# Performance work log

Measured on AMD Instinct MI355X. Metric: run time of the kernel, lower is better.

Reference implementation:

```python
import jax, jax.numpy as jnp
import numpy as np

EPS = 1e-8
PHI = (1 + 5 ** 0.5) / 2
B, S, D, H, L, O = 8, 2048, 256, 512, 3, 1
NH = 4
HD = H // NH


def setup_inputs() -> dict:
    key = jax.random.key(0)
    ks = jax.random.split(key, 12)
    g = lambda k, shape, s=0.02: jax.random.normal(k, shape, dtype=jnp.float32) * s
    # Fibonacci modular spiral embedding (fixed, requires_grad=False in torch)
    idx = jnp.arange(D, dtype=jnp.float32)
    r = (PHI * idx) % 1.0
    th = 2 * jnp.pi * r
    phase_emb = jnp.stack([r * jnp.cos(th), r * jnp.sin(th)], axis=1)  # [D,2]
    return dict(
        x=jax.random.normal(ks[0], (B, S, D), dtype=jnp.float32),
        proj_w=g(ks[1], (D, D), 0.06), proj_b=jnp.zeros((D,), jnp.float32),
        phase_emb=phase_emb,
        hebb_w=g(ks[2], (H, 2), 0.5),
        attn_in_w=g(ks[3], (L, 3 * H, H)), attn_in_b=jnp.zeros((L, 3 * H), jnp.float32),
        attn_out_w=g(ks[4], (L, H, H)), attn_out_b=jnp.zeros((L, H), jnp.float32),
        ff1_w=g(ks[5], (L, 4 * H, H)), ff1_b=jnp.zeros((L, 4 * H), jnp.float32),
        ff2_w=g(ks[6], (L, H, 4 * H)), ff2_b=jnp.zeros((L, H), jnp.float32),
        ln1_w=jnp.ones((L, H), jnp.float32), ln1_b=jnp.zeros((L, H), jnp.float32),
        ln2_w=jnp.ones((L, H), jnp.float32), ln2_b=jnp.zeros((L, H), jnp.float32),
        normA_w=jnp.ones((H,), jnp.float32), normA_b=jnp.zeros((H,), jnp.float32),
        normB_w=jnp.ones((H // 2,), jnp.float32), normB_b=jnp.zeros((H // 2,), jnp.float32),
        p1_w=g(ks[7], (H // 2, H), 0.04), p1_b=jnp.zeros((H // 2,), jnp.float32),
        p2_w=g(ks[8], (O, H // 2), 0.06), p2_b=jnp.zeros((O,), jnp.float32),
    )


def _ln(x, w, b, eps=1e-5):
    m = x.mean(-1, keepdims=True)
    v = ((x - m) ** 2).mean(-1, keepdims=True)
    return (x - m) * jax.lax.rsqrt(v + eps) * w + b


def _diffuse(psi, mask, dt, steps):
    # Norm-preserving RK2 integration of d(psi)/dt = mask@psi - psi
    def force(state):
        return jnp.einsum('bij,bjd->bid', mask, state) - state

    def step(p, _):
        r = jnp.linalg.norm(p, axis=-1, keepdims=True)
        k1 = force(p)
        ps = p + dt * k1
        ps = ps * (r / (jnp.linalg.norm(ps, axis=-1, keepdims=True) + EPS))
        k2 = force(ps)
        pn = p + 0.5 * dt * (k1 + k2)
        pn = pn * (r / (jnp.linalg.norm(pn, axis=-1, keepdims=True) + EPS))
        return pn, None

    psi, _ = jax.lax.scan(step, psi, None, length=steps)
    return psi


def _forward(x, proj_w, proj_b, phase_emb, hebb_w, attn_in_w, attn_in_b,
             attn_out_w, attn_out_b, ff1_w, ff1_b, ff2_w, ff2_b,
             ln1_w, ln1_b, ln2_w, ln2_b, normA_w, normA_b, normB_w, normB_b,
             p1_w, p1_b, p2_w, p2_b):
    b, s, _ = x.shape
    # PhaseHebbianEmbedder: project then map to 2D phase coords, unit-normalize
    xp = x @ proj_w.T + proj_b                               # [B,S,D]
    pc = jnp.einsum('bsd,dt->bst', xp, phase_emb)            # [B,S,2]
    psi = pc / (jnp.linalg.norm(pc, axis=-1, keepdims=True) + EPS)
    mask = jnp.broadcast_to(jnp.eye(s, dtype=x.dtype), (b, s, s))  # [B,S,S]
    psi = _diffuse(psi, mask, 0.1, 3)
    psi = _diffuse(psi, mask, 0.05, 4)
    A = jnp.einsum('bsd,btd->bst', psi, psi)                 # [B,S,S]
    final_psi = psi[:, -1]                                   # [B,2]
    h = (final_psi @ hebb_w.T)[:, None, :]                   # [B,1,H]
    for l in range(attn_in_w.shape[0]):
        qkv = h @ attn_in_w[l].T + attn_in_b[l]
        q, k, v = jnp.split(qkv, 3, axis=-1)
        hd = lambda t: t.reshape(b, -1, NH, HD).transpose(0, 2, 1, 3)
        q, k, v = hd(q), hd(k), hd(v)
        sc = jnp.einsum('bhqd,bhkd->bhqk', q, k) / jnp.sqrt(jnp.float32(HD))
        att = jax.nn.softmax(sc, axis=-1)
        o = jnp.einsum('bhqk,bhkd->bhqd', att, v).transpose(0, 2, 1, 3).reshape(b, -1, H)
        o = o @ attn_out_w[l].T + attn_out_b[l]
        h = _ln(h + o, ln1_w[l], ln1_b[l])
        ff = jax.nn.silu(h @ ff1_w[l].T + ff1_b[l]) @ ff2_w[l].T + ff2_b[l]
        h = _ln(h + ff, ln2_w[l], ln2_b[l])
    h = _ln(h[:, 0, :], normA_w, normA_b)
    p = jax.nn.silu(h @ p1_w.T + p1_b)
    p = _ln(p, normB_w, normB_b)
    preds = p @ p2_w.T + p2_b                                # [B,O]
    return preds, A, mask, psi


def reference(x, proj_w, proj_b, phase_emb, hebb_w, attn_in_w, attn_in_b,
              attn_out_w, attn_out_b, ff1_w, ff1_b, ff2_w, ff2_b,
              ln1_w, ln1_b, ln2_w, ln2_b, normA_w, normA_b, normB_w, normB_b,
              p1_w, p1_b, p2_w, p2_b):
    return _forward(x, proj_w, proj_b, phase_emb, hebb_w, attn_in_w, attn_in_b,
                    attn_out_w, attn_out_b, ff1_w, ff1_b, ff2_w, ff2_b,
                    ln1_w, ln1_b, ln2_w, ln2_b, normA_w, normA_b,
                    normB_w, normB_b, p1_w, p1_b, p2_w, p2_b)
```

## Files before the change

### kernel.cpp

```cpp
#include <hip/hip_runtime.h>
#include <hip/hip_bf16.h>

#define BB 8
#define SS 2048
#define DD 256
#define HH 512
#define LL 3

__global__ void compute_M(const float* __restrict__ pw, const float* __restrict__ pb,
                          const float* __restrict__ pe, float* __restrict__ Mc)
{
    int tid = threadIdx.x;
    int k = tid >> 2;
    int sub = tid & 3;
    float a0 = 0.f, a1 = 0.f;
    #pragma unroll 8
    for (int d = sub * 64; d < sub * 64 + 64; ++d) {
        float w = pw[d * DD + k];
        a0 += w * pe[2 * d];
        a1 += w * pe[2 * d + 1];
    }
    a0 += __shfl_xor(a0, 1); a0 += __shfl_xor(a0, 2);
    a1 += __shfl_xor(a1, 1); a1 += __shfl_xor(a1, 2);
    if (sub == 0) {
        Mc[2 * k] = a0;
        Mc[2 * k + 1] = a1;
    }
    if (tid == 0) {
        float c0 = 0.f, c1 = 0.f;
        #pragma unroll 4
        for (int d = 0; d < DD; ++d) {
            c0 += pb[d] * pe[2 * d];
            c1 += pb[d] * pe[2 * d + 1];
        }
        Mc[512] = c0;
        Mc[513] = c1;
    }
}

__global__ void psi_kernel(const float* __restrict__ x, const float* __restrict__ Mc,
                           float* __restrict__ psi)
{
    __shared__ float sM[516];
    int tid = threadIdx.x;
    for (int i = tid; i < 514; i += 256) sM[i] = Mc[i];
    __syncthreads();

    int sub = tid & 3;
    int rloc = tid >> 2;
    int rid = blockIdx.x * 64 + rloc;
    const float4* xr = reinterpret_cast<const float4*>(x + (size_t)rid * DD);
    float a0 = 0.f, a1 = 0.f;
    #pragma unroll
    for (int i = sub; i < DD / 4; i += 4) {
        float4 v = xr[i];
        int k2 = i * 8;
        a0 += v.x * sM[k2]     + v.y * sM[k2 + 2] + v.z * sM[k2 + 4] + v.w * sM[k2 + 6];
        a1 += v.x * sM[k2 + 1] + v.y * sM[k2 + 3] + v.z * sM[k2 + 5] + v.w * sM[k2 + 7];
    }
    a0 += __shfl_xor(a0, 1); a0 += __shfl_xor(a0, 2);
    a1 += __shfl_xor(a1, 1); a1 += __shfl_xor(a1, 2);

    if (sub == 0) {
        a0 += sM[512];
        a1 += sM[513];
        float n = sqrtf(a0 * a0 + a1 * a1);
        float scale = 1.f / (n + 1e-8f);
        float r = n * scale;
        #pragma unroll
        for (int it = 0; it < 7; ++it) {
            float f = r / (r + 1e-8f);
            scale *= f;
            r *= f;
        }
        float2 pv;
        pv.x = a0 * scale;
        pv.y = a1 * scale;
        *reinterpret_cast<float2*>(psi + (size_t)rid * 2) = pv;
    }
}

__global__ void h0_kernel(const float* __restrict__ psi, const float* __restrict__ hebb,
                          float* __restrict__ h0)
{
    int b = blockIdx.x;
    int j = threadIdx.x;
    float2 pv = *reinterpret_cast<const float2*>(psi + ((size_t)b * SS + SS - 1) * 2);
    h0[(size_t)b * HH + j] = pv.x * hebb[2 * j] + pv.y * hebb[2 * j + 1];
}

__global__ void a_mask_kernel(const float* __restrict__ psi,
                              float* __restrict__ A, float* __restrict__ M)
{
    int blk = blockIdx.x;
    int b = blk >> 11, i = blk & (SS - 1);
    int tid = threadIdx.x;
    float2 pi = *reinterpret_cast<const float2*>(psi + (size_t)blk * 2);
    #pragma unroll
    for (int c = 0; c < 2; ++c) {
        int j0 = c * 1024 + tid * 4;
        const float4* pr = reinterpret_cast<const float4*>(psi + ((size_t)b * SS + j0) * 2);
        float4 q0 = pr[0], q1 = pr[1];
        float4 o;
        o.x = pi.x * q0.x + pi.y * q0.y;
        o.y = pi.x * q0.z + pi.y * q0.w;
        o.z = pi.x * q1.x + pi.y * q1.y;
        o.w = pi.x * q1.z + pi.y * q1.w;
        size_t rb = (size_t)blk * SS + j0;
        *reinterpret_cast<float4*>(A + rb) = o;
        float4 m;
        m.x = (i == j0    ) ? 1.f : 0.f;
        m.y = (i == j0 + 1) ? 1.f : 0.f;
        m.z = (i == j0 + 2) ? 1.f : 0.f;
        m.w = (i == j0 + 3) ? 1.f : 0.f;
        *reinterpret_cast<float4*>(M + rb) = m;
    }
}

__global__ void head_mm(const float* __restrict__ X, int K,
                        const float* __restrict__ xlnw, const float* __restrict__ xlnb,
                        const float* __restrict__ xln2w, const float* __restrict__ xln2b,
                        const float* __restrict__ W, const float* __restrict__ bias,
                        const float* __restrict__ res,
                        const float* __restrict__ reslnw, const float* __restrict__ reslnb,
                        float* __restrict__ out, int J, int G, int act)
{
    extern __shared__ float sX[];
    __shared__ float s_m[8], s_r[8], s_rm[8], s_rr[8];
    const int tid = threadIdx.x;
    const int row = tid >> 5, lane = tid & 31;
    const bool doLN = (xlnw != nullptr);
    const bool doRLN = (res != nullptr) && (reslnw != nullptr);

    if (doLN) {
        float s = 0.f, ss = 0.f;
        for (int k = lane; k < K; k += 32) {
            float v = X[row * K + k];
            s += v; ss += v * v;
        }
        for (int d = 16; d; d >>= 1) { s += __shfl_down(s, d); ss += __shfl_down(ss, d); }
        if (lane == 0) {
            float m = s / K;
            s_m[row] = m;
            s_r[row] = rsqrtf(ss / K - m * m + 1e-5f);
        }
    }
    if (doRLN) {
        float s = 0.f, ss = 0.f;
        for (int k = lane; k < J; k += 32) {
            float v = res[row * J + k];
            s += v; ss += v * v;
        }
        for (int d = 16; d; d >>= 1) { s += __shfl_down(s, d); ss += __shfl_down(ss, d); }
        if (lane == 0) {
            float m = s / J;
            s_rm[row] = m;
            s_rr[row] = rsqrtf(ss / J - m * m + 1e-5f);
        }
    }
    __syncthreads();

    if (doLN) {
        for (int idx = tid; idx < 8 * K; idx += 256) {
            int b = idx / K, k = idx - b * K;
            sX[idx] = (X[idx] - s_m[b]) * s_r[b] * xlnw[k] + xlnb[k];
        }
        __syncthreads();
        if (xln2w) {
            float s = 0.f, ss = 0.f;
            for (int k = lane; k < K; k += 32) {
                float v = sX[row * K + k];
                s += v; ss += v * v;
            }
            for (int d = 16; d; d >>= 1) { s += __shfl_down(s, d); ss += __shfl_down(ss, d); }
            if (lane == 0) {
                float m = s / K;
                s_m[row] = m;
                s_r[row] = rsqrtf(ss / K - m * m + 1e-5f);
            }
            __syncthreads();
            for (int idx = tid; idx < 8 * K; idx += 256) {
                int b = idx / K, k = idx - b * K;
                sX[idx] = (sX[idx] - s_m[b]) * s_r[b] * xln2w[k] + xln2b[k];
            }
            __syncthreads();
        }
    }

    const float* __restrict__ Xp = doLN ? (const float*)sX : X;
    const int g = tid & (G - 1);
    const int jj = tid / G;
    const int j = blockIdx.x * (256 / G) + jj;

    float acc[8] = {0.f, 0.f, 0.f, 0.f, 0.f, 0.f, 0.f, 0.f};
    if (j < J) {
        const float4* W4 = reinterpret_cast<const float4*>(W + (size_t)j * K);
        const int K4 = K >> 2;
        for (int i4 = g; i4 < K4; i4 += G) {
            float4 w4 = W4[i4];
            int k = i4 << 2;
            #pragma unroll
            for (int b = 0; b < 8; ++b) {
                float4 xv = *reinterpret_cast<const float4*>(Xp + b * K + k);
                acc[b] = fmaf(w4.x, xv.x, acc[b]);
                acc[b] = fmaf(w4.y, xv.y, acc[b]);
                acc[b] = fmaf(w4.z, xv.z, acc[b]);
                acc[b] = fmaf(w4.w, xv.w, acc[b]);
            }
        }
    }
    for (int d = G >> 1; d; d >>= 1) {
        #pragma unroll
        for (int b = 0; b < 8; ++b) acc[b] += __shfl_down(acc[b], d);
    }
    if (g == 0 && j < J) {
        float bs = bias ? bias[j] : 0.f;
        #pragma unroll
        for (int b = 0; b < 8; ++b) {
            float v = acc[b] + bs;
            if (act) v = v / (1.f + expf(-v));
            if (res) {
                float rv = res[(size_t)b * J + j];
                if (reslnw) rv = (rv - s_rm[b]) * s_rr[b] * reslnw[j] + reslnb[j];
                v += rv;
            }
            out[(size_t)b * J + j] = v;
        }
    }
}

extern "C" void kernel_launch(void* const* d_in, const int* in_sizes, int n_in,
                              void* d_out, int out_size, void* d_ws, size_t ws_size,
                              hipStream_t stream)
{
    const float* x      = (const float*)d_in[0];
    const float* proj_w = (const float*)d_in[1];
    const float* proj_b = (const float*)d_in[2];
    const float* pe     = (const float*)d_in[3];
    const float* hebb   = (const float*)d_in[4];
    const float* ai_w   = (const float*)d_in[5];
    const float* ai_b   = (const float*)d_in[6];
    const float* ao_w   = (const float*)d_in[7];
    const float* ao_b   = (const float*)d_in[8];
    const float* f1_w   = (const float*)d_in[9];
    const float* f1_b   = (const float*)d_in[10];
    const float* f2_w   = (const float*)d_in[11];
    const float* f2_b   = (const float*)d_in[12];
    const float* ln1w   = (const float*)d_in[13];
    const float* ln1b   = (const float*)d_in[14];
    const float* ln2w   = (const float*)d_in[15];
    const float* ln2b   = (const float*)d_in[16];
    const float* nAw    = (const float*)d_in[17];
    const float* nAb    = (const float*)d_in[18];
    const float* nBw    = (const float*)d_in[19];
    const float* nBb    = (const float*)d_in[20];
    const float* p1w    = (const float*)d_in[21];
    const float* p1b    = (const float*)d_in[22];
    const float* p2w    = (const float*)d_in[23];
    const float* p2b    = (const float*)d_in[24];

    float* out   = (float*)d_out;
    float* preds = out;
    float* A     = out + 8;
    float* Mask  = out + 8 + (size_t)BB * SS * SS;
    float* Psi   = out + 8 + (size_t)2 * BB * SS * SS;

    float* ws = (float*)d_ws;
    float* Mc = ws;
    float* T  = ws + 640;
    float* V  = ws + 4736;
    float* T1 = ws + 8832;
    float* F  = ws + 12928;
    float* P  = ws + 29312;

    compute_M<<<1, 1024, 0, stream>>>(proj_w, proj_b, pe, Mc);
    psi_kernel<<<(BB * SS) / 64, 256, 0, stream>>>(x, Mc, Psi);
    h0_kernel<<<BB, HH, 0, stream>>>(Psi, hebb, T);
    a_mask_kernel<<<BB * SS, 256, 0, stream>>>(Psi, A, Mask);

    for (int l = 0; l < LL; ++l) {
        const float* pxw = l ? ln2w + (l - 1) * HH : nullptr;
        const float* pxb = l ? ln2b + (l - 1) * HH : nullptr;
        head_mm<<<64, 256, (pxw ? 8 * HH * 4 : 0), stream>>>(
            T, HH, pxw, pxb, nullptr, nullptr,
            ai_w + ((size_t)l * 3 * HH + 2 * HH) * HH, ai_b + l * 3 * HH + 2 * HH,
            nullptr, nullptr, nullptr, V, HH, 32, 0);
        head_mm<<<64, 256, 0, stream>>>(
            V, HH, nullptr, nullptr, nullptr, nullptr,
            ao_w + (size_t)l * HH * HH, ao_b + l * HH,
            T, pxw, pxb, T1, HH, 32, 0);
        head_mm<<<128, 256, 8 * HH * 4, stream>>>(
            T1, HH, ln1w + l * HH, ln1b + l * HH, nullptr, nullptr,
            f1_w + (size_t)l * 4 * HH * HH, f1_b + l * 4 * HH,
            nullptr, nullptr, nullptr, F, 4 * HH, 16, 1);
        head_mm<<<128, 256, 0, stream>>>(
            F, 4 * HH, nullptr, nullptr, nullptr, nullptr,
            f2_w + (size_t)l * HH * 4 * HH, f2_b + l * HH,
            T1, ln1w + l * HH, ln1b + l * HH, T, HH, 64, 0);
    }
    head_mm<<<32, 256, 8 * HH * 4, stream>>>(
        T, HH, ln2w + 2 * HH, ln2b + 2 * HH, nAw, nAb,
        p1w, p1b, nullptr, nullptr, nullptr, P, HH / 2, 32, 1);
    head_mm<<<1, 256, 8 * (HH / 2) * 4, stream>>>(
        P, HH / 2, nBw, nBb, nullptr, nullptr,
        p2w, p2b, nullptr, nullptr, nullptr, preds, 1, 32, 0);
}
```

Measured before the change: 249.4 us.

## Spread A/mask row writes across head kernels as extra blocks

The standalone A/mask kernel is removed. Its 16384 rows are split into chunks of about 1092 rows, and each chunk runs as extra blocks appended to the h0 kernel and to every small head matmul launch. This lets the bandwidth-bound writes overlap the latency-bound tiny matmuls. psi_kernel now uses one wave per row with wave-wide shuffles, and compute_M reduces through shared memory. The risk is that the extra blocks delay the matmul blocks on the critical path.

```diff
diff --git a/kernel.cpp b/kernel.cpp
--- a/kernel.cpp
+++ b/kernel.cpp
@@ -6,95 +6,14 @@
 #define DD 256
 #define HH 512
 #define LL 3
-
-__global__ void compute_M(const float* __restrict__ pw, const float* __restrict__ pb,
-                          const float* __restrict__ pe, float* __restrict__ Mc)
+#define NROWS (BB * SS)
+
+__device__ __forceinline__ void amask_row(const float* __restrict__ psi,
+                                          float* __restrict__ A, float* __restrict__ M,
+                                          int blk)
 {
     int tid = threadIdx.x;
-    int k = tid >> 2;
-    int sub = tid & 3;
-    float a0 = 0.f, a1 = 0.f;
-    #pragma unroll 8
-    for (int d = sub * 64; d < sub * 64 + 64; ++d) {
-        float w = pw[d * DD + k];
-        a0 += w * pe[2 * d];
-        a1 += w * pe[2 * d + 1];
-    }
-    a0 += __shfl_xor(a0, 1); a0 += __shfl_xor(a0, 2);
-    a1 += __shfl_xor(a1, 1); a1 += __shfl_xor(a1, 2);
-    if (sub == 0) {
-        Mc[2 * k] = a0;
-        Mc[2 * k + 1] = a1;
-    }
-    if (tid == 0) {
-        float c0 = 0.f, c1 = 0.f;
-        #pragma unroll 4
-        for (int d = 0; d < DD; ++d) {
-            c0 += pb[d] * pe[2 * d];
-            c1 += pb[d] * pe[2 * d + 1];
-        }
-        Mc[512] = c0;
-        Mc[513] = c1;
-    }
-}
-
-__global__ void psi_kernel(const float* __restrict__ x, const float* __restrict__ Mc,
-                           float* __restrict__ psi)
-{
-    __shared__ float sM[516];
-    int tid = threadIdx.x;
-    for (int i = tid; i < 514; i += 256) sM[i] = Mc[i];
-    __syncthreads();
-
-    int sub = tid & 3;
-    int rloc = tid >> 2;
-    int rid = blockIdx.x * 64 + rloc;
-    const float4* xr = reinterpret_cast<const float4*>(x + (size_t)rid * DD);
-    float a0 = 0.f, a1 = 0.f;
-    #pragma unroll
-    for (int i = sub; i < DD / 4; i += 4) {
-        float4 v = xr[i];
-        int k2 = i * 8;
-        a0 += v.x * sM[k2]     + v.y * sM[k2 + 2] + v.z * sM[k2 + 4] + v.w * sM[k2 + 6];
-        a1 += v.x * sM[k2 + 1] + v.y * sM[k2 + 3] + v.z * sM[k2 + 5] + v.w * sM[k2 + 7];
-    }
-    a0 += __shfl_xor(a0, 1); a0 += __shfl_xor(a0, 2);
-    a1 += __shfl_xor(a1, 1); a1 += __shfl_xor(a1, 2);
-
-    if (sub == 0) {
-        a0 += sM[512];
-        a1 += sM[513];
-        float n = sqrtf(a0 * a0 + a1 * a1);
-        float scale = 1.f / (n + 1e-8f);
-        float r = n * scale;
-        #pragma unroll
-        for (int it = 0; it < 7; ++it) {
-            float f = r / (r + 1e-8f);
-            scale *= f;
-            r *= f;
-        }
-        float2 pv;
-        pv.x = a0 * scale;
-        pv.y = a1 * scale;
-        *reinterpret_cast<float2*>(psi + (size_t)rid * 2) = pv;
-    }
-}
-
-__global__ void h0_kernel(const float* __restrict__ psi, const float* __restrict__ hebb,
-                          float* __restrict__ h0)
-{
-    int b = blockIdx.x;
-    int j = threadIdx.x;
-    float2 pv = *reinterpret_cast<const float2*>(psi + ((size_t)b * SS + SS - 1) * 2);
-    h0[(size_t)b * HH + j] = pv.x * hebb[2 * j] + pv.y * hebb[2 * j + 1];
-}
-
-__global__ void a_mask_kernel(const float* __restrict__ psi,
-                              float* __restrict__ A, float* __restrict__ M)
-{
-    int blk = blockIdx.x;
     int b = blk >> 11, i = blk & (SS - 1);
-    int tid = threadIdx.x;
     float2 pi = *reinterpret_cast<const float2*>(psi + (size_t)blk * 2);
     #pragma unroll
     for (int c = 0; c < 2; ++c) {
@@ -117,14 +36,116 @@
     }
 }
 
+__global__ void compute_M(const float* __restrict__ pw, const float* __restrict__ pb,
+                          const float* __restrict__ pe, float* __restrict__ Mc)
+{
+    __shared__ float s0[4][256], s1[4][256];
+    int tid = threadIdx.x;
+    int k = tid & 255;
+    int sub = tid >> 8;
+    float a0 = 0.f, a1 = 0.f;
+    #pragma unroll 8
+    for (int d = sub * 64; d < sub * 64 + 64; ++d) {
+        float w = pw[d * DD + k];
+        a0 += w * pe[2 * d];
+        a1 += w * pe[2 * d + 1];
+    }
+    s0[sub][k] = a0;
+    s1[sub][k] = a1;
+    __syncthreads();
+    if (tid < 256) {
+        Mc[2 * tid]     = s0[0][tid] + s0[1][tid] + s0[2][tid] + s0[3][tid];
+        Mc[2 * tid + 1] = s1[0][tid] + s1[1][tid] + s1[2][tid] + s1[3][tid];
+    }
+    if (tid < 64) {
+        float c0 = 0.f, c1 = 0.f;
+        for (int d = tid; d < DD; d += 64) {
+            c0 += pb[d] * pe[2 * d];
+            c1 += pb[d] * pe[2 * d + 1];
+        }
+        #pragma unroll
+        for (int dd = 32; dd; dd >>= 1) {
+            c0 += __shfl_xor(c0, dd);
+            c1 += __shfl_xor(c1, dd);
+        }
+        if (tid == 0) { Mc[512] = c0; Mc[513] = c1; }
+    }
+}
+
+__global__ void psi_kernel(const float* __restrict__ x, const float* __restrict__ Mc,
+                           float* __restrict__ psi)
+{
+    int tid = threadIdx.x;
+    int wave = tid >> 6, lane = tid & 63;
+    const float4* Mc4 = reinterpret_cast<const float4*>(Mc);
+    float4 mA = Mc4[lane * 2];
+    float4 mB = Mc4[lane * 2 + 1];
+    float c0 = Mc[512], c1 = Mc[513];
+    int base = blockIdx.x * 16 + wave * 4;
+    #pragma unroll
+    for (int it = 0; it < 4; ++it) {
+        int rid = base + it;
+        float4 v = *reinterpret_cast<const float4*>(x + (size_t)rid * DD + lane * 4);
+        float a0 = v.x * mA.x + v.y * mA.z + v.z * mB.x + v.w * mB.z;
+        float a1 = v.x * mA.y + v.y * mA.w + v.z * mB.y + v.w * mB.w;
+        #pragma unroll
+        for (int d = 32; d; d >>= 1) {
+            a0 += __shfl_xor(a0, d);
+            a1 += __shfl_xor(a1, d);
+        }
+        a0 += c0;
+        a1 += c1;
+        float n = sqrtf(a0 * a0 + a1 * a1);
+        float scale = 1.f / (n + 1e-8f);
+        float r = n * scale;
+        #pragma unroll
+        for (int i7 = 0; i7 < 7; ++i7) {
+            float f = r / (r + 1e-8f);
+            scale *= f;
+            r *= f;
+        }
+        if (lane == 0) {
+            float2 pv;
+            pv.x = a0 * scale;
+            pv.y = a1 * scale;
+            *reinterpret_cast<float2*>(psi + (size_t)rid * 2) = pv;
+        }
+    }
+}
+
+__global__ void h0_kernel(const float* __restrict__ psi, const float* __restrict__ hebb,
+                          float* __restrict__ h0,
+                          float* __restrict__ Ao, float* __restrict__ Mo, int arow0)
+{
+    int bid = blockIdx.x;
+    if (bid >= BB) {
+        int r = arow0 + (bid - BB);
+        if (r < NROWS) amask_row(psi, Ao, Mo, r);
+        return;
+    }
+    float2 pv = *reinterpret_cast<const float2*>(psi + ((size_t)bid * SS + SS - 1) * 2);
+    for (int j = threadIdx.x; j < HH; j += blockDim.x)
+        h0[(size_t)bid * HH + j] = pv.x * hebb[2 * j] + pv.y * hebb[2 * j + 1];
+}
+
 __global__ void head_mm(const float* __restrict__ X, int K,
                         const float* __restrict__ xlnw, const float* __restrict__ xlnb,
                         const float* __restrict__ xln2w, const float* __restrict__ xln2b,
                         const float* __restrict__ W, const float* __restrict__ bias,
                         const float* __restrict__ res,
                         const float* __restrict__ reslnw, const float* __restrict__ reslnb,
-                        float* __restrict__ out, int J, int G, int act)
-{
+                        float* __restrict__ out, int J, int G, int act,
+                        const float* __restrict__ psi,
+                        float* __restrict__ Ao, float* __restrict__ Mo,
+                        int mmBlocks, int arow0)
+{
+    const int bid = blockIdx.x;
+    if (bid >= mmBlocks) {
+        int r = arow0 + (bid - mmBlocks);
+        if (r < NROWS) amask_row(psi, Ao, Mo, r);
+        return;
+    }
+
     extern __shared__ float sX[];
     __shared__ float s_m[8], s_r[8], s_rm[8], s_rr[8];
     const int tid = threadIdx.x;
@@ -190,7 +211,7 @@
     const float* __restrict__ Xp = doLN ? (const float*)sX : X;
     const int g = tid & (G - 1);
     const int jj = tid / G;
-    const int j = blockIdx.x * (256 / G) + jj;
+    const int j = bid * (256 / G) + jj;
 
     float acc[8] = {0.f, 0.f, 0.f, 0.f, 0.f, 0.f, 0.f, 0.f};
     if (j < J) {
@@ -274,34 +295,64 @@
     float* P  = ws + 29312;
 
     compute_M<<<1, 1024, 0, stream>>>(proj_w, proj_b, pe, Mc);
-    psi_kernel<<<(BB * SS) / 64, 256, 0, stream>>>(x, Mc, Psi);
-    h0_kernel<<<BB, HH, 0, stream>>>(Psi, hebb, T);
-    a_mask_kernel<<<BB * SS, 256, 0, stream>>>(Psi, A, Mask);
+    psi_kernel<<<NROWS / 16, 256, 0, stream>>>(x, Mc, Psi);
+
+    int ci = 0, arow = 0;
+    auto nextq = [&]() { int q = 1092 + (ci < 4 ? 1 : 0); ++ci; return q; };
+
+    {
+        int q = nextq();
+        h0_kernel<<<BB + q, 256, 0, stream>>>(Psi, hebb, T, A, Mask, arow);
+        arow += q;
+    }
 
     for (int l = 0; l < LL; ++l) {
         const float* pxw = l ? ln2w + (l - 1) * HH : nullptr;
         const float* pxb = l ? ln2b + (l - 1) * HH : nullptr;
-        head_mm<<<64, 256, (pxw ? 8 * HH * 4 : 0), stream>>>(
+        int q;
+        q = nextq();
+        head_mm<<<64 + q, 256, (pxw ? 8 * HH * 4 : 0), stream>>>(
             T, HH, pxw, pxb, nullptr, nullptr,
             ai_w + ((size_t)l * 3 * HH + 2 * HH) * HH, ai_b + l * 3 * HH + 2 * HH,
-            nullptr, nullptr, nullptr, V, HH, 32, 0);
-        head_mm<<<64, 256, 0, stream>>>(
+            nullptr, nullptr, nullptr, V, HH, 32, 0,
+            Psi, A, Mask, 64, arow);
+        arow += q;
+        q = nextq();
+        head_mm<<<64 + q, 256, 0, stream>>>(
             V, HH, nullptr, nullptr, nullptr, nullptr,
             ao_w + (size_t)l * HH * HH, ao_b + l * HH,
-            T, pxw, pxb, T1, HH, 32, 0);
-        head_mm<<<128, 256, 8 * HH * 4, stream>>>(
+            T, pxw, pxb, T1, HH, 32, 0,
+            Psi, A, Mask, 64, arow);
+        arow += q;
+        q = nextq();
+        head_mm<<<128 + q, 256, 8 * HH * 4, stream>>>(
             T1, HH, ln1w + l * HH, ln1b + l * HH, nullptr, nullptr,
             f1_w + (size_t)l * 4 * HH * HH, f1_b + l * 4 * HH,
-            nullptr, nullptr, nullptr, F, 4 * HH, 16, 1);
-        head_mm<<<128, 256, 0, stream>>>(
+            nullptr, nullptr, nullptr, F, 4 * HH, 16, 1,
+            Psi, A, Mask, 128, arow);
+        arow += q;
+        q = nextq();
+        head_mm<<<128 + q, 256, 0, stream>>>(
             F, 4 * HH, nullptr, nullptr, nullptr, nullptr,
             f2_w + (size_t)l * HH * 4 * HH, f2_b + l * HH,
-            T1, ln1w + l * HH, ln1b + l * HH, T, HH, 64, 0);
-    }
-    head_mm<<<32, 256, 8 * HH * 4, stream>>>(
-        T, HH, ln2w + 2 * HH, ln2b + 2 * HH, nAw, nAb,
-        p1w, p1b, nullptr, nullptr, nullptr, P, HH / 2, 32, 1);
-    head_mm<<<1, 256, 8 * (HH / 2) * 4, stream>>>(
-        P, HH / 2, nBw, nBb, nullptr, nullptr,
-        p2w, p2b, nullptr, nullptr, nullptr, preds, 1, 32, 0);
-}
+            T1, ln1w + l * HH, ln1b + l * HH, T, HH, 64, 0,
+            Psi, A, Mask, 128, arow);
+        arow += q;
+    }
+    {
+        int q = nextq();
+        head_mm<<<32 + q, 256, 8 * HH * 4, stream>>>(
+            T, HH, ln2w + 2 * HH, ln2b + 2 * HH, nAw, nAb,
+            p1w, p1b, nullptr, nullptr, nullptr, P, HH / 2, 32, 1,
+            Psi, A, Mask, 32, arow);
+        arow += q;
+    }
+    {
+        int q = nextq();
+        head_mm<<<1 + q, 256, 8 * (HH / 2) * 4, stream>>>(
+            P, HH / 2, nBw, nBb, nullptr, nullptr,
+            p2w, p2b, nullptr, nullptr, nullptr, preds, 1, 32, 0,
+            Psi, A, Mask, 1, arow);
+        arow += q;
+    }
+}
```

Result: faster. 239.8 us (-3.8%).
